# Kernel optimization log

Measured on AMD Instinct MI355X. Metric: run time of the kernel, lower is better.

Reference implementation:

```python
import jax, jax.numpy as jnp
import numpy as np


def setup_inputs() -> dict:
    key = jax.random.key(0)
    ks = jax.random.split(key, 9)
    V, D, C, B = 100000, 128, 10, 16384
    return {
        "target_w_id": jax.random.randint(ks[0], (B,), 0, V),
        "context_w_ids": jax.random.randint(ks[1], (B, C), 0, V),
        "R": jax.random.normal(ks[2], (V, D), dtype=jnp.float32),
        "M_w": jax.random.normal(ks[3], (2 * D, 2 * D), dtype=jnp.float32) * 0.05,
        "M_b": jax.random.normal(ks[4], (2 * D,), dtype=jnp.float32) * 0.05,
        "U_w": jax.random.normal(ks[5], (D, 2 * D), dtype=jnp.float32) * 0.05,
        "U_b": jax.random.normal(ks[6], (D,), dtype=jnp.float32) * 0.05,
        "W_w": jax.random.normal(ks[7], (D, 2 * D), dtype=jnp.float32) * 0.05,
        "W_b": jax.random.normal(ks[8], (D,), dtype=jnp.float32) * 0.05,
    }


def reference(target_w_id, context_w_ids, R, M_w, M_b, U_w, U_b, W_w, W_b):
    # Gather embeddings: tw [B, D], cw [B, C, D]
    tw = R[target_w_id]
    cw = R[context_w_ids]
    B, C, D = cw.shape
    # Concat context embed with (broadcast) target embed -> [B, C, 2D]
    tw_b = jnp.broadcast_to(tw[:, None, :], (B, C, D))
    stacked = jnp.concatenate([cw, tw_b], axis=-1)
    # Linear M (torch: x @ W.T + b), ReLU, sum over context window -> h [B, 2D]
    proj = jnp.einsum("bcd,ed->bce", stacked, M_w) + M_b
    h = jnp.sum(jax.nn.relu(proj), axis=1)
    posterior_mu = h @ U_w.T + U_b
    posterior_sigma = jax.nn.softplus(h @ W_w.T + W_b)
    return (posterior_mu, posterior_sigma)
```

## Files before the change

kernel.cpp:

```cpp
#include <hip/hip_runtime.h>
#include <hip/hip_bf16.h>

typedef __attribute__((ext_vector_type(8))) short short8;
typedef __attribute__((ext_vector_type(4))) float floatx4;

static __device__ __forceinline__ short f2bf(float f) {
    union { float f; unsigned u; } v; v.f = f;
    unsigned r = v.u + 0x7fffu + ((v.u >> 16) & 1u);
    return (short)(r >> 16);
}
static __device__ __forceinline__ float bf2f(short s) {
    union { unsigned u; float f; } v; v.u = ((unsigned)(unsigned short)s) << 16;
    return v.f;
}

#define C_CTX 10
#define D_EMB 128
#define E_DIM 256

__global__ void prep_main(const float* __restrict__ Mw, const float* __restrict__ Uw,
                          const float* __restrict__ Ww, short* __restrict__ M1f,
                          short* __restrict__ M2f, short* __restrict__ B2f)
{
    int u = blockIdx.x * 256 + threadIdx.x;
    const float* src;
    short* dst;
    if (u < 8192) {
        int f = u & 4095;
        int l = f & 63, kc = (f >> 6) & 3, grp = f >> 8;
        int e = grp * 16 + (l & 15);
        int k = kc * 32 + (l >> 4) * 8 + ((u < 4096) ? 0 : 128);
        src = Mw + (size_t)e * E_DIM + k;
        dst = ((u < 4096) ? M1f : M2f) + (size_t)f * 8;
    } else {
        int f = u - 8192;
        int l = f & 63, ni = (f >> 6) & 3, kc = (f >> 8) & 7, w = f >> 11;
        int e = w * 64 + ni * 16 + (l & 15);
        int k = kc * 32 + (l >> 4) * 8;
        src = (e < 128) ? (Uw + (size_t)e * E_DIM + k)
                        : (Ww + (size_t)(e - 128) * E_DIM + k);
        dst = B2f + (size_t)f * 8;
    }
    float4 x = *(const float4*)src;
    float4 y = *(const float4*)(src + 4);
    short8 o;
    o[0]=f2bf(x.x); o[1]=f2bf(x.y); o[2]=f2bf(x.z); o[3]=f2bf(x.w);
    o[4]=f2bf(y.x); o[5]=f2bf(y.y); o[6]=f2bf(y.z); o[7]=f2bf(y.w);
    *(short8*)dst = o;
}

__global__ __launch_bounds__(256, 4)
void k_gt2(const float* __restrict__ R, const short* __restrict__ M1f,
           const short* __restrict__ M2f, const float* __restrict__ Mb,
           const int* __restrict__ tgt, short* __restrict__ G,
           float* __restrict__ Tt, int V, int NG)
{
    __shared__ __align__(16) short buf[64 * 264];
    __shared__ int tids[64];
    const int t = threadIdx.x, w = t >> 6, l = t & 63;
    const bool isG = (int)blockIdx.x < NG;
    const int r0 = (isG ? blockIdx.x : (blockIdx.x - NG)) * 64;

    if (!isG && t < 64) tids[t] = tgt[r0 + t];
    if (!isG) __syncthreads();

    #pragma unroll
    for (int i = 0; i < 4; ++i) {
        int fa = t + i * 256;
        int li = fa & 63, frag = fa >> 6;
        int kc = frag >> 2, mi = frag & 3;
        int r = mi * 16 + (li & 15);
        int k = kc * 32 + (li >> 4) * 8;
        int gr;
        if (isG) { gr = r0 + r; if (gr >= V) gr = V - 1; }
        else     { gr = tids[r]; }
        const float* s = R + (size_t)gr * D_EMB + k;
        float4 x = *(const float4*)s;
        float4 y = *(const float4*)(s + 4);
        short8 v;
        v[0]=f2bf(x.x); v[1]=f2bf(x.y); v[2]=f2bf(x.z); v[3]=f2bf(x.w);
        v[4]=f2bf(y.x); v[5]=f2bf(y.y); v[6]=f2bf(y.z); v[7]=f2bf(y.w);
        *(short8*)&buf[fa * 8] = v;
    }
    __syncthreads();

    const short* Bf = isG ? M1f : M2f;
    floatx4 acc[4][4];
    #pragma unroll
    for (int mi = 0; mi < 4; ++mi)
        #pragma unroll
        for (int ni = 0; ni < 4; ++ni)
            acc[mi][ni] = (floatx4){0.f, 0.f, 0.f, 0.f};

    #pragma unroll
    for (int kc = 0; kc < 4; ++kc) {
        short8 afr[4], bfr[4];
        #pragma unroll
        for (int mi = 0; mi < 4; ++mi)
            afr[mi] = *(const short8*)&buf[((kc * 4 + mi) * 64 + l) * 8];
        #pragma unroll
        for (int ni = 0; ni < 4; ++ni)
            bfr[ni] = *(const short8*)(Bf + (((size_t)(w * 4 + ni) * 4 + kc) * 64 + l) * 8);
        #pragma unroll
        for (int mi = 0; mi < 4; ++mi)
            #pragma unroll
            for (int ni = 0; ni < 4; ++ni)
                acc[mi][ni] = __builtin_amdgcn_mfma_f32_16x16x32_bf16(afr[mi], bfr[ni], acc[mi][ni], 0, 0, 0);
    }

    if (isG) {
        __syncthreads();
        #pragma unroll
        for (int mi = 0; mi < 4; ++mi)
            #pragma unroll
            for (int ni = 0; ni < 4; ++ni) {
                int col = w * 64 + ni * 16 + (l & 15);
                #pragma unroll
                for (int j = 0; j < 4; ++j) {
                    int row = mi * 16 + (l >> 4) * 4 + j;
                    buf[row * 264 + col] = f2bf(acc[mi][ni][j]);
                }
            }
        __syncthreads();
        #pragma unroll
        for (int i = 0; i < 8; ++i) {
            int u = t + i * 256;
            int row = u >> 5, c8 = (u & 31) * 8;
            int gr = r0 + row;
            if (gr < V)
                *(short8*)(G + (size_t)gr * 256 + c8) = *(const short8*)&buf[row * 264 + c8];
        }
    } else {
        #pragma unroll
        for (int mi = 0; mi < 4; ++mi)
            #pragma unroll
            for (int ni = 0; ni < 4; ++ni) {
                int col = w * 64 + ni * 16 + (l & 15);
                float mb = Mb[col];
                #pragma unroll
                for (int j = 0; j < 4; ++j) {
                    int row = mi * 16 + (l >> 4) * 4 + j;
                    Tt[(size_t)(r0 + row) * E_DIM + col] = acc[mi][ni][j] + mb;
                }
            }
    }
}

__global__ __launch_bounds__(256, 4)
void k_hh(const int* __restrict__ ctx, const short* __restrict__ G,
          const float* __restrict__ Tt, const short* __restrict__ B2f,
          const float* __restrict__ Ub, const float* __restrict__ Wb,
          float* __restrict__ out, int Bsz)
{
    __shared__ __align__(16) short hfr[8 * 64 * 8];
    __shared__ int ids[16 * C_CTX];
    const int t = threadIdx.x, w = t >> 6, l = t & 63;
    const int b0 = blockIdx.x * 16;

    if (t < 16 * C_CTX) ids[t] = ctx[(size_t)b0 * C_CTX + t];
    __syncthreads();

    const int hw = l >> 5;
    const int i5 = l & 31;
    const int kcc = i5 & 7, sub = i5 >> 3;
    const int c8 = kcc * 32 + sub * 8;

    #pragma unroll
    for (int p = 0; p < 2; ++p) {
        int bl = p * 8 + w * 2 + hw;
        const float* tp = Tt + (size_t)(b0 + bl) * E_DIM + c8;
        float4 x = *(const float4*)tp;
        float4 y = *(const float4*)(tp + 4);
        float tv[8] = {x.x, x.y, x.z, x.w, y.x, y.y, y.z, y.w};
        float acc[8] = {0.f, 0.f, 0.f, 0.f, 0.f, 0.f, 0.f, 0.f};
        #pragma unroll
        for (int c = 0; c < C_CTX; ++c) {
            short8 g = *(const short8*)(G + (size_t)ids[bl * C_CTX + c] * E_DIM + c8);
            #pragma unroll
            for (int j = 0; j < 8; ++j)
                acc[j] += fmaxf(bf2f(g[j]) + tv[j], 0.f);
        }
        int sp = (sub * 16 + bl) ^ kcc;
        short8 o;
        #pragma unroll
        for (int j = 0; j < 8; ++j) o[j] = f2bf(acc[j]);
        *(short8*)&hfr[(kcc * 64 + sp) * 8] = o;
    }
    __syncthreads();

    floatx4 acc2[4];
    #pragma unroll
    for (int ni = 0; ni < 4; ++ni)
        acc2[ni] = (floatx4){0.f, 0.f, 0.f, 0.f};

    #pragma unroll
    for (int kc = 0; kc < 8; ++kc) {
        short8 afr = *(const short8*)&hfr[(kc * 64 + (l ^ kc)) * 8];
        short8 bfr[4];
        #pragma unroll
        for (int ni = 0; ni < 4; ++ni)
            bfr[ni] = *(const short8*)(B2f + ((((size_t)w * 8 + kc) * 4 + ni) * 64 + l) * 8);
        #pragma unroll
        for (int ni = 0; ni < 4; ++ni)
            acc2[ni] = __builtin_amdgcn_mfma_f32_16x16x32_bf16(afr, bfr[ni], acc2[ni], 0, 0, 0);
    }

    #pragma unroll
    for (int ni = 0; ni < 4; ++ni) {
        int col = w * 64 + ni * 16 + (l & 15);
        #pragma unroll
        for (int j = 0; j < 4; ++j) {
            int r = b0 + (l >> 4) * 4 + j;
            float v = acc2[ni][j];
            if (col < 128) {
                out[(size_t)r * 128 + col] = v + Ub[col];
            } else {
                float xx = v + Wb[col - 128];
                float sp = fmaxf(xx, 0.f) + log1pf(expf(-fabsf(xx)));
                out[(size_t)Bsz * 128 + (size_t)r * 128 + (col - 128)] = sp;
            }
        }
    }
}

extern "C" void kernel_launch(void* const* d_in, const int* in_sizes, int n_in,
                              void* d_out, int out_size, void* d_ws, size_t ws_size,
                              hipStream_t stream)
{
    const int*   tgt = (const int*)d_in[0];
    const int*   ctx = (const int*)d_in[1];
    const float* R   = (const float*)d_in[2];
    const float* Mw  = (const float*)d_in[3];
    const float* Mb  = (const float*)d_in[4];
    const float* Uw  = (const float*)d_in[5];
    const float* Ub  = (const float*)d_in[6];
    const float* Ww  = (const float*)d_in[7];
    const float* Wb  = (const float*)d_in[8];
    float* out = (float*)d_out;
    const int Bsz = in_sizes[0];
    const int Vn  = in_sizes[2] / D_EMB;

    char* ws = (char*)d_ws;
    size_t offG   = 0;
    size_t offT   = offG + (size_t)Vn * 512;
    size_t offM1f = offT + (size_t)Bsz * 1024;
    size_t offM2f = offM1f + 65536;
    size_t offB2f = offM2f + 65536;

    short* G   = (short*)(ws + offG);
    float* Tt  = (float*)(ws + offT);
    short* M1f = (short*)(ws + offM1f);
    short* M2f = (short*)(ws + offM2f);
    short* B2f = (short*)(ws + offB2f);

    const int NG = (Vn + 63) / 64;
    const int NT = Bsz / 64;

    prep_main<<<64, 256, 0, stream>>>(Mw, Uw, Ww, M1f, M2f, B2f);
    k_gt2<<<NG + NT, 256, 0, stream>>>(R, M1f, M2f, Mb, tgt, G, Tt, Vn, NG);
    k_hh<<<Bsz / 16, 256, 0, stream>>>(ctx, G, Tt, B2f, Ub, Wb, out, Bsz);
}
```

Before: 65.00 us.

## Halve block tiles, store target projection in bf16, raise occupancy

Row tiles in the projection kernel shrink from 64 to 32 rows and batch tiles in the context-sum kernel shrink from 16 to 8. Launch bounds are raised to 6 and 8 blocks, so there are more blocks and higher occupancy. The target projection T is now stored as bf16 through the same shared-memory path as G, which halves its write and read traffic. In exchange, half the MFMA rows in k_hh are wasted, and the bf16 rounding of T plus bias adds precision loss.

```diff
diff --git a/kernel.cpp b/kernel.cpp
--- a/kernel.cpp
+++ b/kernel.cpp
@@ -49,26 +49,26 @@
     *(short8*)dst = o;
 }
 
-__global__ __launch_bounds__(256, 4)
+__global__ __launch_bounds__(256, 6)
 void k_gt2(const float* __restrict__ R, const short* __restrict__ M1f,
            const short* __restrict__ M2f, const float* __restrict__ Mb,
            const int* __restrict__ tgt, short* __restrict__ G,
-           float* __restrict__ Tt, int V, int NG)
-{
-    __shared__ __align__(16) short buf[64 * 264];
-    __shared__ int tids[64];
+           short* __restrict__ Ttb, int V, int NG)
+{
+    __shared__ __align__(16) short buf[32 * 264];
+    __shared__ int tids[32];
     const int t = threadIdx.x, w = t >> 6, l = t & 63;
     const bool isG = (int)blockIdx.x < NG;
-    const int r0 = (isG ? blockIdx.x : (blockIdx.x - NG)) * 64;
-
-    if (!isG && t < 64) tids[t] = tgt[r0 + t];
+    const int r0 = (isG ? blockIdx.x : (blockIdx.x - NG)) * 32;
+
+    if (!isG && t < 32) tids[t] = tgt[r0 + t];
     if (!isG) __syncthreads();
 
     #pragma unroll
-    for (int i = 0; i < 4; ++i) {
+    for (int i = 0; i < 2; ++i) {
         int fa = t + i * 256;
         int li = fa & 63, frag = fa >> 6;
-        int kc = frag >> 2, mi = frag & 3;
+        int kc = frag >> 1, mi = frag & 1;
         int r = mi * 16 + (li & 15);
         int k = kc * 32 + (li >> 4) * 8;
         int gr;
@@ -85,101 +85,89 @@
     __syncthreads();
 
     const short* Bf = isG ? M1f : M2f;
-    floatx4 acc[4][4];
-    #pragma unroll
-    for (int mi = 0; mi < 4; ++mi)
+    floatx4 acc[2][4];
+    #pragma unroll
+    for (int mi = 0; mi < 2; ++mi)
         #pragma unroll
         for (int ni = 0; ni < 4; ++ni)
             acc[mi][ni] = (floatx4){0.f, 0.f, 0.f, 0.f};
 
     #pragma unroll
     for (int kc = 0; kc < 4; ++kc) {
-        short8 afr[4], bfr[4];
-        #pragma unroll
-        for (int mi = 0; mi < 4; ++mi)
-            afr[mi] = *(const short8*)&buf[((kc * 4 + mi) * 64 + l) * 8];
+        short8 afr[2], bfr[4];
+        #pragma unroll
+        for (int mi = 0; mi < 2; ++mi)
+            afr[mi] = *(const short8*)&buf[((kc * 2 + mi) * 64 + l) * 8];
         #pragma unroll
         for (int ni = 0; ni < 4; ++ni)
             bfr[ni] = *(const short8*)(Bf + (((size_t)(w * 4 + ni) * 4 + kc) * 64 + l) * 8);
         #pragma unroll
-        for (int mi = 0; mi < 4; ++mi)
+        for (int mi = 0; mi < 2; ++mi)
             #pragma unroll
             for (int ni = 0; ni < 4; ++ni)
                 acc[mi][ni] = __builtin_amdgcn_mfma_f32_16x16x32_bf16(afr[mi], bfr[ni], acc[mi][ni], 0, 0, 0);
     }
-
-    if (isG) {
-        __syncthreads();
-        #pragma unroll
-        for (int mi = 0; mi < 4; ++mi)
+    __syncthreads();
+
+    #pragma unroll
+    for (int mi = 0; mi < 2; ++mi)
+        #pragma unroll
+        for (int ni = 0; ni < 4; ++ni) {
+            int col = w * 64 + ni * 16 + (l & 15);
+            float bias = isG ? 0.f : Mb[col];
             #pragma unroll
-            for (int ni = 0; ni < 4; ++ni) {
-                int col = w * 64 + ni * 16 + (l & 15);
-                #pragma unroll
-                for (int j = 0; j < 4; ++j) {
-                    int row = mi * 16 + (l >> 4) * 4 + j;
-                    buf[row * 264 + col] = f2bf(acc[mi][ni][j]);
-                }
+            for (int j = 0; j < 4; ++j) {
+                int row = mi * 16 + (l >> 4) * 4 + j;
+                buf[row * 264 + col] = f2bf(acc[mi][ni][j] + bias);
             }
-        __syncthreads();
-        #pragma unroll
-        for (int i = 0; i < 8; ++i) {
-            int u = t + i * 256;
-            int row = u >> 5, c8 = (u & 31) * 8;
-            int gr = r0 + row;
-            if (gr < V)
-                *(short8*)(G + (size_t)gr * 256 + c8) = *(const short8*)&buf[row * 264 + c8];
         }
-    } else {
-        #pragma unroll
-        for (int mi = 0; mi < 4; ++mi)
-            #pragma unroll
-            for (int ni = 0; ni < 4; ++ni) {
-                int col = w * 64 + ni * 16 + (l & 15);
-                float mb = Mb[col];
-                #pragma unroll
-                for (int j = 0; j < 4; ++j) {
-                    int row = mi * 16 + (l >> 4) * 4 + j;
-                    Tt[(size_t)(r0 + row) * E_DIM + col] = acc[mi][ni][j] + mb;
-                }
-            }
-    }
-}
-
-__global__ __launch_bounds__(256, 4)
+    __syncthreads();
+
+    short* dst = isG ? G : Ttb;
+    #pragma unroll
+    for (int i = 0; i < 4; ++i) {
+        int u = t + i * 256;
+        int row = u >> 5, c8 = (u & 31) * 8;
+        int gr = r0 + row;
+        if (!isG || gr < V)
+            *(short8*)(dst + (size_t)gr * 256 + c8) = *(const short8*)&buf[row * 264 + c8];
+    }
+}
+
+__global__ __launch_bounds__(256, 8)
 void k_hh(const int* __restrict__ ctx, const short* __restrict__ G,
-          const float* __restrict__ Tt, const short* __restrict__ B2f,
+          const short* __restrict__ Ttb, const short* __restrict__ B2f,
           const float* __restrict__ Ub, const float* __restrict__ Wb,
           float* __restrict__ out, int Bsz)
 {
     __shared__ __align__(16) short hfr[8 * 64 * 8];
-    __shared__ int ids[16 * C_CTX];
+    __shared__ int ids[8 * C_CTX];
     const int t = threadIdx.x, w = t >> 6, l = t & 63;
-    const int b0 = blockIdx.x * 16;
-
-    if (t < 16 * C_CTX) ids[t] = ctx[(size_t)b0 * C_CTX + t];
+    const int b0 = blockIdx.x * 8;
+
+    if (t < 8 * C_CTX) ids[t] = ctx[(size_t)b0 * C_CTX + t];
     __syncthreads();
 
     const int hw = l >> 5;
     const int i5 = l & 31;
     const int kcc = i5 & 7, sub = i5 >> 3;
     const int c8 = kcc * 32 + sub * 8;
-
-    #pragma unroll
-    for (int p = 0; p < 2; ++p) {
-        int bl = p * 8 + w * 2 + hw;
-        const float* tp = Tt + (size_t)(b0 + bl) * E_DIM + c8;
-        float4 x = *(const float4*)tp;
-        float4 y = *(const float4*)(tp + 4);
-        float tv[8] = {x.x, x.y, x.z, x.w, y.x, y.y, y.z, y.w};
-        float acc[8] = {0.f, 0.f, 0.f, 0.f, 0.f, 0.f, 0.f, 0.f};
-        #pragma unroll
-        for (int c = 0; c < C_CTX; ++c) {
-            short8 g = *(const short8*)(G + (size_t)ids[bl * C_CTX + c] * E_DIM + c8);
-            #pragma unroll
-            for (int j = 0; j < 8; ++j)
-                acc[j] += fmaxf(bf2f(g[j]) + tv[j], 0.f);
-        }
+    const int bl = w * 2 + hw;
+
+    short8 tr = *(const short8*)(Ttb + (size_t)(b0 + bl) * E_DIM + c8);
+    float tv[8], acc[8];
+    #pragma unroll
+    for (int j = 0; j < 8; ++j) { tv[j] = bf2f(tr[j]); acc[j] = 0.f; }
+
+    #pragma unroll
+    for (int c = 0; c < C_CTX; ++c) {
+        short8 g = *(const short8*)(G + (size_t)ids[bl * C_CTX + c] * E_DIM + c8);
+        #pragma unroll
+        for (int j = 0; j < 8; ++j)
+            acc[j] += fmaxf(bf2f(g[j]) + tv[j], 0.f);
+    }
+
+    {
         int sp = (sub * 16 + bl) ^ kcc;
         short8 o;
         #pragma unroll
@@ -210,14 +198,17 @@
         int col = w * 64 + ni * 16 + (l & 15);
         #pragma unroll
         for (int j = 0; j < 4; ++j) {
-            int r = b0 + (l >> 4) * 4 + j;
-            float v = acc2[ni][j];
-            if (col < 128) {
-                out[(size_t)r * 128 + col] = v + Ub[col];
-            } else {
-                float xx = v + Wb[col - 128];
-                float sp = fmaxf(xx, 0.f) + log1pf(expf(-fabsf(xx)));
-                out[(size_t)Bsz * 128 + (size_t)r * 128 + (col - 128)] = sp;
+            int rr = (l >> 4) * 4 + j;
+            if (rr < 8) {
+                int r = b0 + rr;
+                float v = acc2[ni][j];
+                if (col < 128) {
+                    out[(size_t)r * 128 + col] = v + Ub[col];
+                } else {
+                    float xx = v + Wb[col - 128];
+                    float sp = fmaxf(xx, 0.f) + log1pf(expf(-fabsf(xx)));
+                    out[(size_t)Bsz * 128 + (size_t)r * 128 + (col - 128)] = sp;
+                }
             }
         }
     }
@@ -243,20 +234,20 @@
     char* ws = (char*)d_ws;
     size_t offG   = 0;
     size_t offT   = offG + (size_t)Vn * 512;
-    size_t offM1f = offT + (size_t)Bsz * 1024;
+    size_t offM1f = offT + (size_t)Bsz * 512;
     size_t offM2f = offM1f + 65536;
     size_t offB2f = offM2f + 65536;
 
     short* G   = (short*)(ws + offG);
-    float* Tt  = (float*)(ws + offT);
+    short* Ttb = (short*)(ws + offT);
     short* M1f = (short*)(ws + offM1f);
     short* M2f = (short*)(ws + offM2f);
     short* B2f = (short*)(ws + offB2f);
 
-    const int NG = (Vn + 63) / 64;
-    const int NT = Bsz / 64;
+    const int NG = (Vn + 31) / 32;
+    const int NT = Bsz / 32;
 
     prep_main<<<64, 256, 0, stream>>>(Mw, Uw, Ww, M1f, M2f, B2f);
-    k_gt2<<<NG + NT, 256, 0, stream>>>(R, M1f, M2f, Mb, tgt, G, Tt, Vn, NG);
-    k_hh<<<Bsz / 16, 256, 0, stream>>>(ctx, G, Tt, B2f, Ub, Wb, out, Bsz);
-}
+    k_gt2<<<NG + NT, 256, 0, stream>>>(R, M1f, M2f, Mb, tgt, G, Ttb, Vn, NG);
+    k_hh<<<Bsz / 8, 256, 0, stream>>>(ctx, G, Ttb, B2f, Ub, Wb, out, Bsz);
+}
```

Measured after the change: 102.1 us. 57.0% more time.
